# Kernel optimization log

Hardware: AMD Instinct MI355X
Metric: run time of the kernel (lower is better)

The kernel has to match this reference:

```python
import jax, jax.numpy as jnp
import numpy as np

N, P, D = 65536, 2048, 512


def setup_inputs() -> dict:
    key = jax.random.key(0)
    k1, k2 = jax.random.split(key)
    embeddings = jax.random.normal(k1, (N, D), dtype=jnp.float32)
    # torch.rand -> uniform [0, 1)
    prototypes = jax.random.uniform(k2, (P, D), dtype=jnp.float32)
    return {"embeddings": embeddings, "prototypes": prototypes}


def reference(embeddings, prototypes):
    # Euclidean distance to prototypes via the quadratic-expansion GEMM trick:
    # torch.norm(embeddings[:,None,:] - prototypes[None,:,:], dim=-1)).
    x_sq = jnp.sum(embeddings * embeddings, axis=-1, keepdims=True)      # [N, 1]
    p_sq = jnp.sum(prototypes * prototypes, axis=-1)[None, :]            # [1, P]
    cross = jnp.einsum("nd,pd->np", embeddings, prototypes)             # [N, P]
    d2 = jnp.maximum(x_sq - 2.0 * cross + p_sq, 0.0)
    dists = jnp.sqrt(d2)
    return -dists  # [N, P]
```

## Files before the change

### kernel.cpp

```cpp
#include <hip/hip_runtime.h>
#include <hip/hip_bf16.h>
#include <cstdint>
#include <math.h>

#define N_EMB   65536
#define N_PROTO 2048
#define DIM     512


typedef __bf16 bf16x8 __attribute__((ext_vector_type(8)));
typedef float  f32x4  __attribute__((ext_vector_type(4)));

__device__ inline bf16x8 cvt8(float4 u, float4 v) {
    bf16x8 r;
    r[0] = (__bf16)u.x; r[1] = (__bf16)u.y; r[2] = (__bf16)u.z; r[3] = (__bf16)u.w;
    r[4] = (__bf16)v.x; r[5] = (__bf16)v.y; r[6] = (__bf16)v.z; r[7] = (__bf16)v.w;
    return r;
}
__device__ inline float dot4(float4 a) { return a.x*a.x + a.y*a.y + a.z*a.z + a.w*a.w; }

__global__ __launch_bounds__(256) void fused_kernel(const float* __restrict__ E,
                                                    const float* __restrict__ Pm,
                                                    float* __restrict__ out) {
    __shared__ __align__(16) __bf16 sA[128 * 32];
    __shared__ __align__(16) __bf16 sB[128 * 32];
    __shared__ __align__(16) float ldsXsq[128];
    __shared__ __align__(16) float ldsPsq[128];

    const int tid   = threadIdx.x;
    const int wave  = tid >> 6, lane = tid & 63;
    const int wm    = wave >> 1, wn = wave & 1;
    const int laneM = lane & 15, laneQ = lane >> 4;

    const int rowBase = blockIdx.y * 128;
    const int colBase = blockIdx.x * 128;

    const int rL   = lane >> 1;
    const int h    = lane & 1;
    const int sRow = wave * 32 + rL;
    const float* gA = E  + (size_t)(rowBase + sRow) * DIM + h * 16;
    const float* gB = Pm + (size_t)(colBase + sRow) * DIM + h * 16;
    __bf16* wA = sA + sRow * 32 + h * 16;
    __bf16* wB = sB + sRow * 32 + h * 16;

    float4 a0 = *(const float4*)(gA + 0), a1 = *(const float4*)(gA + 4);
    float4 a2 = *(const float4*)(gA + 8), a3 = *(const float4*)(gA + 12);
    float4 b0 = *(const float4*)(gB + 0), b1 = *(const float4*)(gB + 4);
    float4 b2 = *(const float4*)(gB + 8), b3 = *(const float4*)(gB + 12);

    float ssqA = 0.0f, ssqB = 0.0f;
    f32x4 acc[4][4] = {};

    #pragma unroll 1
    for (int kt = 0; kt < DIM / 32; ++kt) {
        ssqA += dot4(a0) + dot4(a1) + dot4(a2) + dot4(a3);
        ssqB += dot4(b0) + dot4(b1) + dot4(b2) + dot4(b3);
        *(bf16x8*)(wA)     = cvt8(a0, a1);
        *(bf16x8*)(wA + 8) = cvt8(a2, a3);
        *(bf16x8*)(wB)     = cvt8(b0, b1);
        *(bf16x8*)(wB + 8) = cvt8(b2, b3);
        __syncthreads();

        if (kt != DIM / 32 - 1) {
            const float* nA = gA + (kt + 1) * 32;
            const float* nB = gB + (kt + 1) * 32;
            a0 = *(const float4*)(nA + 0); a1 = *(const float4*)(nA + 4);
            a2 = *(const float4*)(nA + 8); a3 = *(const float4*)(nA + 12);
            b0 = *(const float4*)(nB + 0); b1 = *(const float4*)(nB + 4);
            b2 = *(const float4*)(nB + 8); b3 = *(const float4*)(nB + 12);
        }

        bf16x8 af[4], bfr[4];
        #pragma unroll
        for (int mi = 0; mi < 4; ++mi)
            af[mi] = *(const bf16x8*)(sA + (wm*64 + mi*16 + laneM) * 32 + laneQ * 8);
        #pragma unroll
        for (int ni = 0; ni < 4; ++ni)
            bfr[ni] = *(const bf16x8*)(sB + (wn*64 + ni*16 + laneM) * 32 + laneQ * 8);
        #pragma unroll
        for (int mi = 0; mi < 4; ++mi)
            #pragma unroll
            for (int ni = 0; ni < 4; ++ni)
                acc[mi][ni] = __builtin_amdgcn_mfma_f32_16x16x32_bf16(af[mi], bfr[ni], acc[mi][ni], 0, 0, 0);
        __syncthreads();
    }

    {
        const float vA = ssqA + __shfl_xor(ssqA, 1);
        const float vB = ssqB + __shfl_xor(ssqB, 1);
        if (h == 0) { ldsXsq[sRow] = vA; ldsPsq[sRow] = vB; }
    }
    __syncthreads();

    #pragma unroll
    for (int mi = 0; mi < 4; ++mi) {
        const int rm0 = wm*64 + mi*16 + laneQ*4;
        const float4 xs = *(const float4*)(ldsXsq + rm0);
        #pragma unroll
        for (int ni = 0; ni < 4; ++ni) {
            const int cn = wn*64 + ni*16 + laneM;
            const float pq = ldsPsq[cn];
            float* o = out + (size_t)(rowBase + rm0) * N_PROTO + (colBase + cn);
            const f32x4 c = acc[mi][ni];
            o[0 * N_PROTO] = -sqrtf(fmaxf(xs.x - 2.0f * c[0] + pq, 0.0f));
            o[1 * N_PROTO] = -sqrtf(fmaxf(xs.y - 2.0f * c[1] + pq, 0.0f));
            o[2 * N_PROTO] = -sqrtf(fmaxf(xs.z - 2.0f * c[2] + pq, 0.0f));
            o[3 * N_PROTO] = -sqrtf(fmaxf(xs.w - 2.0f * c[3] + pq, 0.0f));
        }
    }
}

extern "C" void kernel_launch(void* const* d_in, const int* in_sizes, int n_in,
                              void* d_out, int out_size, void* d_ws, size_t ws_size,
                              hipStream_t stream) {
    const float* emb = (const float*)d_in[0];
    const float* pro = (const float*)d_in[1];
    float* out = (float*)d_out;
    (void)d_ws; (void)ws_size; (void)in_sizes; (void)n_in; (void)out_size;

    fused_kernel<<<dim3(N_PROTO / 128, N_EMB / 128), 256, 0, stream>>>(emb, pro, out);
}
```

Measured before the change: 968.3 us.

## Load MFMA fragments directly from global memory, dropping LDS staging and barriers

Each wave now loads its own A and B fragments straight from global memory into registers, converts them to bf16, and feeds them to MFMA. This removes the shared-memory tiles and the two barriers per K step. Row norms are reduced with cross-lane shuffles instead of LDS. Output stores become nontemporal, and launch bounds request 3 blocks per CU. The cost is lost data sharing between waves: each A/B row is now fetched by two waves, which raises L2/global traffic, and loads are strided without software prefetch.

Measured after the change: 1.512 ms. +56.2%, slower.

```diff
diff --git a/kernel.cpp b/kernel.cpp
--- a/kernel.cpp
+++ b/kernel.cpp
@@ -19,93 +19,75 @@
 }
 __device__ inline float dot4(float4 a) { return a.x*a.x + a.y*a.y + a.z*a.z + a.w*a.w; }
 
-__global__ __launch_bounds__(256) void fused_kernel(const float* __restrict__ E,
-                                                    const float* __restrict__ Pm,
-                                                    float* __restrict__ out) {
-    __shared__ __align__(16) __bf16 sA[128 * 32];
-    __shared__ __align__(16) __bf16 sB[128 * 32];
-    __shared__ __align__(16) float ldsXsq[128];
-    __shared__ __align__(16) float ldsPsq[128];
-
+__global__ __launch_bounds__(256, 3) void fused_kernel(const float* __restrict__ E,
+                                                       const float* __restrict__ Pm,
+                                                       float* __restrict__ out) {
     const int tid   = threadIdx.x;
     const int wave  = tid >> 6, lane = tid & 63;
     const int wm    = wave >> 1, wn = wave & 1;
     const int laneM = lane & 15, laneQ = lane >> 4;
 
-    const int rowBase = blockIdx.y * 128;
-    const int colBase = blockIdx.x * 128;
+    const int rowBase = blockIdx.y * 128 + wm * 64;
+    const int colBase = blockIdx.x * 128 + wn * 64;
 
-    const int rL   = lane >> 1;
-    const int h    = lane & 1;
-    const int sRow = wave * 32 + rL;
-    const float* gA = E  + (size_t)(rowBase + sRow) * DIM + h * 16;
-    const float* gB = Pm + (size_t)(colBase + sRow) * DIM + h * 16;
-    __bf16* wA = sA + sRow * 32 + h * 16;
-    __bf16* wB = sB + sRow * 32 + h * 16;
+    const float* pA[4];
+    const float* pB[4];
+    #pragma unroll
+    for (int mi = 0; mi < 4; ++mi)
+        pA[mi] = E  + (size_t)(rowBase + mi * 16 + laneM) * DIM + laneQ * 8;
+    #pragma unroll
+    for (int ni = 0; ni < 4; ++ni)
+        pB[ni] = Pm + (size_t)(colBase + ni * 16 + laneM) * DIM + laneQ * 8;
 
-    float4 a0 = *(const float4*)(gA + 0), a1 = *(const float4*)(gA + 4);
-    float4 a2 = *(const float4*)(gA + 8), a3 = *(const float4*)(gA + 12);
-    float4 b0 = *(const float4*)(gB + 0), b1 = *(const float4*)(gB + 4);
-    float4 b2 = *(const float4*)(gB + 8), b3 = *(const float4*)(gB + 12);
+    f32x4 acc[4][4] = {};
+    float nA[4] = {0.f, 0.f, 0.f, 0.f};
+    float nB[4] = {0.f, 0.f, 0.f, 0.f};
 
-    float ssqA = 0.0f, ssqB = 0.0f;
-    f32x4 acc[4][4] = {};
-
-    #pragma unroll 1
     for (int kt = 0; kt < DIM / 32; ++kt) {
-        ssqA += dot4(a0) + dot4(a1) + dot4(a2) + dot4(a3);
-        ssqB += dot4(b0) + dot4(b1) + dot4(b2) + dot4(b3);
-        *(bf16x8*)(wA)     = cvt8(a0, a1);
-        *(bf16x8*)(wA + 8) = cvt8(a2, a3);
-        *(bf16x8*)(wB)     = cvt8(b0, b1);
-        *(bf16x8*)(wB + 8) = cvt8(b2, b3);
-        __syncthreads();
-
-        if (kt != DIM / 32 - 1) {
-            const float* nA = gA + (kt + 1) * 32;
-            const float* nB = gB + (kt + 1) * 32;
-            a0 = *(const float4*)(nA + 0); a1 = *(const float4*)(nA + 4);
-            a2 = *(const float4*)(nA + 8); a3 = *(const float4*)(nA + 12);
-            b0 = *(const float4*)(nB + 0); b1 = *(const float4*)(nB + 4);
-            b2 = *(const float4*)(nB + 8); b3 = *(const float4*)(nB + 12);
-        }
-
+        const int ko = kt * 32;
         bf16x8 af[4], bfr[4];
         #pragma unroll
-        for (int mi = 0; mi < 4; ++mi)
-            af[mi] = *(const bf16x8*)(sA + (wm*64 + mi*16 + laneM) * 32 + laneQ * 8);
+        for (int mi = 0; mi < 4; ++mi) {
+            const float4 u = *(const float4*)(pA[mi] + ko);
+            const float4 v = *(const float4*)(pA[mi] + ko + 4);
+            nA[mi] += dot4(u) + dot4(v);
+            af[mi] = cvt8(u, v);
+        }
         #pragma unroll
-        for (int ni = 0; ni < 4; ++ni)
-            bfr[ni] = *(const bf16x8*)(sB + (wn*64 + ni*16 + laneM) * 32 + laneQ * 8);
+        for (int ni = 0; ni < 4; ++ni) {
+            const float4 u = *(const float4*)(pB[ni] + ko);
+            const float4 v = *(const float4*)(pB[ni] + ko + 4);
+            nB[ni] += dot4(u) + dot4(v);
+            bfr[ni] = cvt8(u, v);
+        }
         #pragma unroll
         for (int mi = 0; mi < 4; ++mi)
             #pragma unroll
             for (int ni = 0; ni < 4; ++ni)
                 acc[mi][ni] = __builtin_amdgcn_mfma_f32_16x16x32_bf16(af[mi], bfr[ni], acc[mi][ni], 0, 0, 0);
-        __syncthreads();
     }
 
-    {
-        const float vA = ssqA + __shfl_xor(ssqA, 1);
-        const float vB = ssqB + __shfl_xor(ssqB, 1);
-        if (h == 0) { ldsXsq[sRow] = vA; ldsPsq[sRow] = vB; }
+    #pragma unroll
+    for (int i = 0; i < 4; ++i) {
+        nA[i] += __shfl_xor(nA[i], 16); nA[i] += __shfl_xor(nA[i], 32);
+        nB[i] += __shfl_xor(nB[i], 16); nB[i] += __shfl_xor(nB[i], 32);
     }
-    __syncthreads();
 
     #pragma unroll
     for (int mi = 0; mi < 4; ++mi) {
-        const int rm0 = wm*64 + mi*16 + laneQ*4;
-        const float4 xs = *(const float4*)(ldsXsq + rm0);
+        float xs[4];
+        #pragma unroll
+        for (int r = 0; r < 4; ++r) xs[r] = __shfl(nA[mi], laneQ * 4 + r);
         #pragma unroll
         for (int ni = 0; ni < 4; ++ni) {
-            const int cn = wn*64 + ni*16 + laneM;
-            const float pq = ldsPsq[cn];
-            float* o = out + (size_t)(rowBase + rm0) * N_PROTO + (colBase + cn);
+            const float pq = nB[ni];
+            float* o = out + (size_t)(rowBase + mi * 16 + laneQ * 4) * N_PROTO
+                           + (colBase + ni * 16 + laneM);
             const f32x4 c = acc[mi][ni];
-            o[0 * N_PROTO] = -sqrtf(fmaxf(xs.x - 2.0f * c[0] + pq, 0.0f));
-            o[1 * N_PROTO] = -sqrtf(fmaxf(xs.y - 2.0f * c[1] + pq, 0.0f));
-            o[2 * N_PROTO] = -sqrtf(fmaxf(xs.z - 2.0f * c[2] + pq, 0.0f));
-            o[3 * N_PROTO] = -sqrtf(fmaxf(xs.w - 2.0f * c[3] + pq, 0.0f));
+            __builtin_nontemporal_store(-sqrtf(fmaxf(xs[0] - 2.0f * c[0] + pq, 0.0f)), o + 0 * (size_t)N_PROTO);
+            __builtin_nontemporal_store(-sqrtf(fmaxf(xs[1] - 2.0f * c[1] + pq, 0.0f)), o + 1 * (size_t)N_PROTO);
+            __builtin_nontemporal_store(-sqrtf(fmaxf(xs[2] - 2.0f * c[2] + pq, 0.0f)), o + 2 * (size_t)N_PROTO);
+            __builtin_nontemporal_store(-sqrtf(fmaxf(xs[3] - 2.0f * c[3] + pq, 0.0f)), o + 3 * (size_t)N_PROTO);
         }
     }
 }
```
